# Kernel optimization log

Hardware: AMD Instinct MI355X
Metric: run time of the kernel (lower is better)

The kernel has to match this reference:

```python
import jax, jax.numpy as jnp
import numpy as np

N_NODES = 10000
N_EDGES = 80000
IN_DIM = 768
HID = 256
HEADS = 8
NEG_SLOPE = 0.2


def setup_inputs() -> dict:
    key = jax.random.key(0)
    ks = jax.random.split(key, 12)
    s = 0.02
    x = jax.random.normal(ks[0], (N_NODES, IN_DIM), dtype=jnp.float32)
    edge_index = jax.random.randint(ks[1], (2, N_EDGES), 0, N_NODES, dtype=jnp.int64)
    W1 = jax.random.normal(ks[2], (IN_DIM, HEADS * HID), dtype=jnp.float32) * s
    a_src1 = jax.random.normal(ks[3], (HEADS, HID), dtype=jnp.float32) * s
    a_dst1 = jax.random.normal(ks[4], (HEADS, HID), dtype=jnp.float32) * s
    b1 = jnp.zeros((HEADS * HID,), dtype=jnp.float32)
    W2 = jax.random.normal(ks[5], (HEADS * HID, HEADS * HID), dtype=jnp.float32) * s
    a_src2 = jax.random.normal(ks[6], (HEADS, HID), dtype=jnp.float32) * s
    a_dst2 = jax.random.normal(ks[7], (HEADS, HID), dtype=jnp.float32) * s
    b2 = jnp.zeros((HID,), dtype=jnp.float32)
    # graph_projection: 256 -> 256
    Wp = jax.random.normal(ks[8], (HID, HID), dtype=jnp.float32) * s
    bp = jnp.zeros((HID,), dtype=jnp.float32)
    return dict(x=x, edge_index=edge_index, W1=W1, a_src1=a_src1, a_dst1=a_dst1,
                b1=b1, W2=W2, a_src2=a_src2, a_dst2=a_dst2, b2=b2, Wp=Wp, bp=bp)


def _gat_conv(x, src, dst, W, a_src, a_dst, b, concat):
    """PyG GATConv (eval mode, self-loops already appended to src/dst)."""
    N = x.shape[0]
    H, C = a_src.shape
    h = (x @ W).reshape(N, H, C)                         # [N,H,C] per-head projection
    alpha_s = jnp.sum(h * a_src[None], axis=-1)           # [N,H]
    alpha_d = jnp.sum(h * a_dst[None], axis=-1)           # [N,H]
    e = jax.nn.leaky_relu(alpha_s[src] + alpha_d[dst], NEG_SLOPE)  # [E,H]
    # segment softmax over incoming edges of each dst node
    m = jax.ops.segment_max(e, dst, num_segments=N)       # [N,H]
    m = jnp.where(jnp.isfinite(m), m, 0.0)
    p = jnp.exp(e - m[dst])
    denom = jax.ops.segment_sum(p, dst, num_segments=N)   # [N,H]
    alpha = p / (denom[dst] + 1e-16)                      # [E,H]
    out = jax.ops.segment_sum(alpha[:, :, None] * h[src], dst, num_segments=N)  # [N,H,C]
    if concat:
        return out.reshape(N, H * C) + b
    return out.mean(axis=1) + b


def reference(x, edge_index, W1, a_src1, a_dst1, b1, W2, a_src2, a_dst2, b2, Wp, bp):
    N = x.shape[0]
    loops = jnp.arange(N, dtype=edge_index.dtype)
    src = jnp.concatenate([edge_index[0], loops])
    dst = jnp.concatenate([edge_index[1], loops])
    h = _gat_conv(x, src, dst, W1, a_src1, a_dst1, b1, concat=True)   # [N, 2048]
    h = jax.nn.elu(h)                                                 # dropout: eval/no-op
    h = _gat_conv(h, src, dst, W2, a_src2, a_dst2, b2, concat=False)  # [N, 256]
    h = h @ Wp + bp
    return jax.nn.relu(h)                                             # dropout: eval/no-op
```

## Files before the change

kernel.cpp:

```cpp
#include <hip/hip_runtime.h>
#include <cstdint>
#include <cstddef>

#define IN_DIM  768
#define NNODES  10000
#define MPAD    10240
#define NEDGES  80000
#define E_TOT   90000
#define HEADS   8
#define HID     256
#define HC      2048
#define NEG_SLOPE 0.2f

#define CVT_BLK  ((MPAD * IN_DIM / 4) / 256)
#define CNT_BLK  ((E_TOT + 255) / 256)
#define T1_BLK   ((HC / 32) * (IN_DIM / 32))
#define T2_BLK   ((HC / 32) * (HC / 32))
#define TP_BLK   ((HID / 32) * (HID / 32))
#define PREP_BLK (CVT_BLK + CNT_BLK + T1_BLK + T2_BLK + TP_BLK)

typedef _Float16 __attribute__((ext_vector_type(8))) f16x8;
typedef float    __attribute__((ext_vector_type(4))) f32x4;

__device__ __forceinline__ int edge_src(const int* __restrict__ ei, int e) {
    return (e < NEDGES) ? ei[e] : (e - NEDGES);
}
__device__ __forceinline__ int edge_dst(const int* __restrict__ ei, int e) {
    return (e < NEDGES) ? ei[NEDGES + e] : (e - NEDGES);
}

__device__ __forceinline__ void tcvt_body(
    const float* __restrict__ W, _Float16* __restrict__ T,
    int K, int N, int bx, int by, int t)
{
    __shared__ float tile[32][33];
    int tx = t & 31, ty = t >> 5;
#pragma unroll
    for (int q = 0; q < 4; q++)
        tile[ty + q * 8][tx] = W[(size_t)(by * 32 + ty + q * 8) * N + bx * 32 + tx];
    __syncthreads();
#pragma unroll
    for (int q = 0; q < 4; q++) {
        float v = tile[tx][ty + q * 8];
        T[(size_t)(bx * 32 + ty + q * 8) * K + by * 32 + tx] = (_Float16)v;
    }
}

__global__ __launch_bounds__(256) void prep_kernel(
    const float* __restrict__ x, _Float16* __restrict__ xh,
    const int* __restrict__ ei, int* __restrict__ cnt,
    const float* __restrict__ W1, _Float16* __restrict__ W1t,
    const float* __restrict__ W2, _Float16* __restrict__ W2t,
    const float* __restrict__ Wp, _Float16* __restrict__ Wpt)
{
    int b = blockIdx.x;
    int t = threadIdx.x;
    if (b < CVT_BLK) {
        int i = b * 256 + t;
        size_t e = (size_t)i * 4;
        int r = (int)(e / IN_DIM);
        float4 v = (r < NNODES) ? *(const float4*)(x + e)
                                : make_float4(0.f, 0.f, 0.f, 0.f);
        _Float16 h4[4] = {(_Float16)v.x, (_Float16)v.y, (_Float16)v.z, (_Float16)v.w};
        *(ushort4*)(xh + e) = *(ushort4*)h4;
    } else if (b < CVT_BLK + CNT_BLK) {
        int e = (b - CVT_BLK) * 256 + t;
        if (e < E_TOT) atomicAdd(&cnt[edge_dst(ei, e)], 1);
    } else if (b < CVT_BLK + CNT_BLK + T1_BLK) {
        int idx = b - (CVT_BLK + CNT_BLK);
        tcvt_body(W1, W1t, IN_DIM, HC, idx % (HC / 32), idx / (HC / 32), t);
    } else if (b < CVT_BLK + CNT_BLK + T1_BLK + T2_BLK) {
        int idx = b - (CVT_BLK + CNT_BLK + T1_BLK);
        tcvt_body(W2, W2t, HC, HC, idx % (HC / 32), idx / (HC / 32), t);
    } else {
        int idx = b - (CVT_BLK + CNT_BLK + T1_BLK + T2_BLK);
        tcvt_body(Wp, Wpt, HID, HID, idx % (HID / 32), idx / (HID / 32), t);
    }
}

__global__ void scan_kernel(const int* __restrict__ cnt, int* __restrict__ indptr) {
    __shared__ int sums[1024];
    const int CH = 10;
    int t = threadIdx.x;
    int base = t * CH;
    int s = 0;
#pragma unroll
    for (int i = 0; i < CH; i++) { int idx = base + i; if (idx < NNODES) s += cnt[idx]; }
    sums[t] = s;
    __syncthreads();
    for (int off = 1; off < 1024; off <<= 1) {
        int v = (t >= off) ? sums[t - off] : 0;
        __syncthreads();
        sums[t] += v;
        __syncthreads();
    }
    int run = (t == 0) ? 0 : sums[t - 1];
#pragma unroll
    for (int i = 0; i < CH; i++) {
        int idx = base + i;
        if (idx < NNODES) { indptr[idx] = run; run += cnt[idx]; }
    }
    if (t == 0) indptr[NNODES] = E_TOT;
}

__global__ void scatter_kernel(const int* __restrict__ ei, const int* __restrict__ indptr,
                               int* __restrict__ cur, int* __restrict__ sorted) {
    int e = blockIdx.x * 256 + threadIdx.x;
    if (e < E_TOT) {
        int d = edge_dst(ei, e);
        int pos = atomicAdd(&cur[d], 1);
        sorted[indptr[d] + pos] = e;
    }
}

__global__ __launch_bounds__(512, 2) void gemm8p_kernel(
    const _Float16* __restrict__ A, const _Float16* __restrict__ B,
    _Float16* __restrict__ C, int M, int K, int Nn)
{
    __shared__ __align__(16) _Float16 lds[2][36864];

    const int t = threadIdx.x;
    const int w = t >> 6, lane = t & 63;
    const int fr = lane & 15, q4 = lane >> 4;
    const int wr = w >> 2, wc = w & 3;

    const int nwgx = gridDim.x;
    int wg = blockIdx.y * nwgx + blockIdx.x;
    const int cpx = (nwgx * gridDim.y) >> 3;
    wg = (wg & 7) * cpx + (wg >> 3);
    const int row0 = (wg / nwgx) * 320;
    const int col0 = (wg % nwgx) * 256;

    const int rowt = t >> 3;
    const int scol = ((t & 7) ^ (rowt & 7)) << 3;
    const _Float16* baseA = A + (size_t)(row0 + rowt) * K + scol;
    const _Float16* baseB = B + (size_t)(col0 + rowt) * K + scol;
    const int dstw = w * 512;

    auto stageA = [&](int q, int kel, int bb) {
        __builtin_amdgcn_global_load_lds(
            (const __attribute__((address_space(1))) void*)(baseA + (size_t)q * 64 * K + kel),
            (__attribute__((address_space(3))) void*)&lds[bb][q * 4096 + dstw], 16, 0, 0);
    };
    auto stageB = [&](int q, int kel, int bb) {
        __builtin_amdgcn_global_load_lds(
            (const __attribute__((address_space(1))) void*)(baseB + (size_t)q * 64 * K + kel),
            (__attribute__((address_space(3))) void*)&lds[bb][20480 + q * 4096 + dstw], 16, 0, 0);
    };

    f32x4 acc[2][2][5][2];
#pragma unroll
    for (int qm = 0; qm < 2; qm++)
#pragma unroll
        for (int qn = 0; qn < 2; qn++)
#pragma unroll
            for (int mi = 0; mi < 5; mi++)
#pragma unroll
                for (int ni = 0; ni < 2; ni++)
                    acc[qm][qn][mi][ni] = {0.f, 0.f, 0.f, 0.f};

    f16x8 fa[5][2], fb[2][2];

#define LOADA(BB, QM)                                                           \
    {                                                                           \
        _Pragma("unroll")                                                       \
        for (int mi = 0; mi < 5; mi++) {                                        \
            _Pragma("unroll")                                                   \
            for (int ks = 0; ks < 2; ks++) {                                    \
                int lr = wr * 80 + mi * 16 + fr;                                \
                int sl = ((ks << 2) | q4) ^ (fr & 7);                           \
                fa[mi][ks] = *(const f16x8*)&lds[BB][(QM) * 10240 + (lr << 6) + (sl << 3)]; \
            }                                                                   \
        }                                                                       \
    }
#define LOADB(BB, QN)                                                           \
    {                                                                           \
        _Pragma("unroll")                                                       \
        for (int ni = 0; ni < 2; ni++) {                                        \
            _Pragma("unroll")                                                   \
            for (int ks = 0; ks < 2; ks++) {                                    \
                int lr = wc * 32 + ni * 16 + fr;                                \
                int sl = ((ks << 2) | q4) ^ (fr & 7);                           \
                fb[ni][ks] = *(const f16x8*)&lds[BB][20480 + (QN) * 8192 + (lr << 6) + (sl << 3)]; \
            }                                                                   \
        }                                                                       \
    }

#define PHASE(QM, QN, LOAD_STMT, STAGE_STMT, WAIT_STMT)                         \
    do {                                                                        \
        WAIT_STMT;                                                              \
        __builtin_amdgcn_s_barrier();                                           \
        LOAD_STMT;                                                              \
        STAGE_STMT;                                                             \
        asm volatile("s_waitcnt lgkmcnt(0)" ::: "memory");                      \
        __builtin_amdgcn_sched_barrier(0);                                      \
        __builtin_amdgcn_s_setprio(1);                                          \
        _Pragma("unroll")                                                       \
        for (int ks = 0; ks < 2; ks++) {                                        \
            _Pragma("unroll")                                                   \
            for (int mi = 0; mi < 5; mi++) {                                    \
                _Pragma("unroll")                                               \
                for (int ni = 0; ni < 2; ni++)                                  \
                    acc[QM][QN][mi][ni] = __builtin_amdgcn_mfma_f32_16x16x32_f16(\
                        fa[mi][ks], fb[ni][ks], acc[QM][QN][mi][ni], 0, 0, 0);  \
            }                                                                   \
        }                                                                       \
        __builtin_amdgcn_s_setprio(0);                                          \
        __builtin_amdgcn_sched_barrier(0);                                      \
    } while (0)

#define VM(N) asm volatile("s_waitcnt vmcnt(" #N ")" ::: "memory")

    stageA(0, 0, 0); stageA(1, 0, 0); stageA(2, 0, 0);
    stageB(0, 0, 0); stageB(1, 0, 0);
    stageB(2, 0, 0); stageB(3, 0, 0);
    stageA(3, 0, 0); stageA(4, 0, 0);

    const int nT = K >> 6;
    int t0 = 0;
    for (; t0 < nT - 1; ++t0) {
        int bb = t0 & 1;
        int bn = bb ^ 1;
        int k1 = (t0 + 1) << 6;
        PHASE(0, 0, { LOADA(bb, 0); LOADB(bb, 0); },
              { stageA(0, k1, bn); stageA(1, k1, bn); stageA(2, k1, bn); },
              VM(4));
        PHASE(0, 1, { LOADB(bb, 1); },
              { stageB(0, k1, bn); stageB(1, k1, bn); },
              VM(5));
        PHASE(1, 1, { LOADA(bb, 1); },
              { stageB(2, k1, bn); stageB(3, k1, bn); },
              VM(5));
        PHASE(1, 0, { LOADB(bb, 0); },
              { stageA(3, k1, bn); stageA(4, k1, bn); },
              ((void)0));
    }
    {
        int bb = t0 & 1;
        PHASE(0, 0, { LOADA(bb, 0); LOADB(bb, 0); }, ((void)0), VM(4));
        PHASE(0, 1, { LOADB(bb, 1); },               ((void)0), VM(2));
        PHASE(1, 1, { LOADA(bb, 1); },               ((void)0), VM(0));
        PHASE(1, 0, { LOADB(bb, 0); },               ((void)0), ((void)0));
    }
#undef PHASE
#undef LOADA
#undef LOADB
#undef VM

#pragma unroll
    for (int qm = 0; qm < 2; qm++)
#pragma unroll
        for (int qn = 0; qn < 2; qn++)
#pragma unroll
            for (int mi = 0; mi < 5; mi++) {
                int mb = row0 + qm * 160 + wr * 80 + mi * 16 + q4 * 4;
#pragma unroll
                for (int ni = 0; ni < 2; ni++) {
                    int n = col0 + qn * 128 + wc * 32 + ni * 16 + fr;
#pragma unroll
                    for (int r = 0; r < 4; r++) {
                        int m = mb + r;
                        if (m < M) C[(size_t)m * Nn + n] = (_Float16)acc[qm][qn][mi][ni][r];
                    }
                }
            }
}

template <int EPI>
__global__ __launch_bounds__(256) void mfma_gemm_kernel(
    const _Float16* __restrict__ A, const _Float16* __restrict__ B,
    void* __restrict__ Cout, const float* __restrict__ bias,
    int M, int K, int Nn, int swz)
{
    __shared__ __align__(16) _Float16 sA[2][128 * 32];
    __shared__ __align__(16) _Float16 sB[2][128 * 32];

    int t = threadIdx.x;
    int bx = blockIdx.x, by = blockIdx.y;
    if (swz) {
        int id = by * 16 + bx;
        int xcd = id & 7, slot = id >> 3;
        bx = 2 * xcd + (slot & 1);
        by = slot >> 1;
    }
    int row0 = by * 128;
    int col0 = bx * 128;

    int s0 = t, s1 = t + 256;
    int m0 = s0 >> 2, k0 = (s0 & 3) * 8;
    int m1 = s1 >> 2, k1 = (s1 & 3) * 8;
    const _Float16* a0 = A + (size_t)(row0 + m0) * K + k0;
    const _Float16* a1 = A + (size_t)(row0 + m1) * K + k1;
    const _Float16* b0 = B + (size_t)(col0 + m0) * K + k0;
    const _Float16* b1 = B + (size_t)(col0 + m1) * K + k1;

    int w = t >> 6, lane = t & 63;
    int wm = (w & 1) * 64, wn = (w >> 1) * 64;
    int fr = lane & 15, quad = lane >> 4;

    auto stage = [&](int kt, int bsel) {
        _Float16* dA0 = &sA[bsel][(w * 64) * 8];
        _Float16* dA1 = &sA[bsel][(w * 64 + 256) * 8];
        _Float16* dB0 = &sB[bsel][(w * 64) * 8];
        _Float16* dB1 = &sB[bsel][(w * 64 + 256) * 8];
        __builtin_amdgcn_global_load_lds(
            (const __attribute__((address_space(1))) void*)(a0 + kt),
            (__attribute__((address_space(3))) void*)dA0, 16, 0, 0);
        __builtin_amdgcn_global_load_lds(
            (const __attribute__((address_space(1))) void*)(a1 + kt),
            (__attribute__((address_space(3))) void*)dA1, 16, 0, 0);
        __builtin_amdgcn_global_load_lds(
            (const __attribute__((address_space(1))) void*)(b0 + kt),
            (__attribute__((address_space(3))) void*)dB0, 16, 0, 0);
        __builtin_amdgcn_global_load_lds(
            (const __attribute__((address_space(1))) void*)(b1 + kt),
            (__attribute__((address_space(3))) void*)dB1, 16, 0, 0);
    };

    f32x4 acc[4][4];
#pragma unroll
    for (int i = 0; i < 4; i++)
#pragma unroll
        for (int j = 0; j < 4; j++) acc[i][j] = {0.f, 0.f, 0.f, 0.f};

    const int nIt = K / 32;
    stage(0, 0);
    __syncthreads();

    for (int it = 0; it < nIt; ++it) {
        int cb = it & 1;
        if (it + 1 < nIt) stage((it + 1) * 32, cb ^ 1);

        f16x8 fa[4], fb[4];
#pragma unroll
        for (int i = 0; i < 4; i++) {
            fa[i] = *(const f16x8*)&sA[cb][(wm + i * 16 + fr) * 32 + quad * 8];
            fb[i] = *(const f16x8*)&sB[cb][(wn + i * 16 + fr) * 32 + quad * 8];
        }
#pragma unroll
        for (int i = 0; i < 4; i++)
#pragma unroll
            for (int j = 0; j < 4; j++)
                acc[i][j] = __builtin_amdgcn_mfma_f32_16x16x32_f16(fa[i], fb[j], acc[i][j], 0, 0, 0);

        if (it + 1 < nIt) __syncthreads();
    }

    if (EPI == 0) {
        _Float16* C = (_Float16*)Cout;
#pragma unroll
        for (int i = 0; i < 4; i++) {
            int mbase = row0 + wm + i * 16 + quad * 4;
#pragma unroll
            for (int j = 0; j < 4; j++) {
                int n = col0 + wn + j * 16 + fr;
#pragma unroll
                for (int r = 0; r < 4; r++) {
                    int m = mbase + r;
                    if (m < M) C[(size_t)m * Nn + n] = (_Float16)acc[i][j][r];
                }
            }
        }
    } else {
        float* C = (float*)Cout;
        float bv[4];
#pragma unroll
        for (int j = 0; j < 4; j++) bv[j] = bias[col0 + wn + j * 16 + fr];
#pragma unroll
        for (int i = 0; i < 4; i++) {
            int mbase = row0 + wm + i * 16 + quad * 4;
#pragma unroll
            for (int j = 0; j < 4; j++) {
                int n = col0 + wn + j * 16 + fr;
#pragma unroll
                for (int r = 0; r < 4; r++) {
                    int m = mbase + r;
                    if (m < M) C[(size_t)m * Nn + n] = fmaxf(acc[i][j][r] + bv[j], 0.f);
                }
            }
        }
    }
}

__global__ __launch_bounds__(256) void attn_kernel(
    const _Float16* __restrict__ H, const float* __restrict__ a_src,
    const float* __restrict__ a_dst, float* __restrict__ as_out,
    float* __restrict__ ad_out)
{
    int n = blockIdx.x;
    int t = threadIdx.x;
    int h = t >> 5, l = t & 31;
    f16x8 hv = *(const f16x8*)&H[(size_t)n * HC + h * HID + l * 8];
    const float* asp = a_src + h * HID + l * 8;
    const float* adp = a_dst + h * HID + l * 8;
    float sa = 0.f, sd = 0.f;
#pragma unroll
    for (int q = 0; q < 8; q++) {
        float v = (float)hv[q];
        sa = fmaf(v, asp[q], sa);
        sd = fmaf(v, adp[q], sd);
    }
#pragma unroll
    for (int o = 16; o > 0; o >>= 1) {
        sa += __shfl_xor(sa, o, 32);
        sd += __shfl_xor(sd, o, 32);
    }
    if (l == 0) { as_out[n * HEADS + h] = sa; ad_out[n * HEADS + h] = sd; }
}

template <int MODE>
__global__ __launch_bounds__(256) void agg_kernel(
    const _Float16* __restrict__ H, const float* __restrict__ as_,
    const float* __restrict__ ad_, const float* __restrict__ bias,
    const int* __restrict__ indptr, const int* __restrict__ sorted,
    const int* __restrict__ ei, _Float16* __restrict__ outh)
{
    __shared__ float m8[HEADS], d8[HEADS], adl[HEADS];
    __shared__ int   srcl[64];
    __shared__ float al[64][HEADS];
    __shared__ float red[HC];

    int n = blockIdx.x;
    int t = threadIdx.x;

    if (n >= NNODES) {
        if (MODE == 0) {
            _Float16 z8[8] = {};
            *(f16x8*)&outh[(size_t)n * HC + t * 8] = *(f16x8*)z8;
        } else {
            outh[(size_t)n * HID + t] = (_Float16)0.f;
        }
        return;
    }

    int start = indptr[n];
    int deg = indptr[n + 1] - start;

    if (t < HEADS) adl[t] = ad_[n * HEADS + t];
    __syncthreads();

    int h = t >> 5, l = t & 31;
    float adh = adl[h];

    float mx = -1e30f;
    for (int j = l; j < deg; j += 32) {
        int e = sorted[start + j];
        int s = edge_src(ei, e);
        float v = as_[s * HEADS + h] + adh;
        v = (v >= 0.f) ? v : NEG_SLOPE * v;
        mx = fmaxf(mx, v);
    }
#pragma unroll
    for (int o = 16; o > 0; o >>= 1) mx = fmaxf(mx, __shfl_xor(mx, o, 32));

    float sm = 0.f;
    for (int j = l; j < deg; j += 32) {
        int e = sorted[start + j];
        int s = edge_src(ei, e);
        float v = as_[s * HEADS + h] + adh;
        v = (v >= 0.f) ? v : NEG_SLOPE * v;
        sm += expf(v - mx);
    }
#pragma unroll
    for (int o = 16; o > 0; o >>= 1) sm += __shfl_xor(sm, o, 32);
    if (l == 0) { m8[h] = mx; d8[h] = sm; }

    int hh = t >> 5, c8 = (t & 31) * 8;
    const size_t hoff = (size_t)hh * HID + c8;
    float acc[8] = {};
    for (int base = 0; base < deg; base += 64) {
        int cntc = min(64, deg - base);
        __syncthreads();
        if (t < cntc) srcl[t] = edge_src(ei, sorted[start + base + t]);
        __syncthreads();
        {
            int j = t & 63, h0 = t >> 6;
            if (j < cntc) {
#pragma unroll
                for (int q = 0; q < 2; q++) {
                    int hx = h0 + q * 4;
                    float v = as_[srcl[j] * HEADS + hx] + adl[hx];
                    v = (v >= 0.f) ? v : NEG_SLOPE * v;
                    al[j][hx] = expf(v - m8[hx]) / (d8[hx] + 1e-16f);
                }
            }
        }
        __syncthreads();
        int jj = 0;
        for (; jj + 3 < cntc; jj += 4) {
            int sx0 = srcl[jj + 0], sx1 = srcl[jj + 1];
            int sx2 = srcl[jj + 2], sx3 = srcl[jj + 3];
            f16x8 h0v = *(const f16x8*)&H[(size_t)sx0 * HC + hoff];
            f16x8 h1v = *(const f16x8*)&H[(size_t)sx1 * HC + hoff];
            f16x8 h2v = *(const f16x8*)&H[(size_t)sx2 * HC + hoff];
            f16x8 h3v = *(const f16x8*)&H[(size_t)sx3 * HC + hoff];
            float a0 = al[jj + 0][hh], a1 = al[jj + 1][hh];
            float a2 = al[jj + 2][hh], a3 = al[jj + 3][hh];
#pragma unroll
            for (int q = 0; q < 8; q++) acc[q] = fmaf(a0, (float)h0v[q], acc[q]);
#pragma unroll
            for (int q = 0; q < 8; q++) acc[q] = fmaf(a1, (float)h1v[q], acc[q]);
#pragma unroll
            for (int q = 0; q < 8; q++) acc[q] = fmaf(a2, (float)h2v[q], acc[q]);
#pragma unroll
            for (int q = 0; q < 8; q++) acc[q] = fmaf(a3, (float)h3v[q], acc[q]);
        }
        for (; jj < cntc; jj++) {
            int s = srcl[jj];
            f16x8 hv = *(const f16x8*)&H[(size_t)s * HC + hoff];
            float a = al[jj][hh];
#pragma unroll
            for (int q = 0; q < 8; q++)
                acc[q] = fmaf(a, (float)hv[q], acc[q]);
        }
    }

    if (MODE == 0) {
        _Float16 o8[8];
#pragma unroll
        for (int q = 0; q < 8; q++) {
            float v = acc[q] + bias[hoff + q];
            v = (v > 0.f) ? v : expm1f(v);
            o8[q] = (_Float16)v;
        }
        *(f16x8*)&outh[(size_t)n * HC + hoff] = *(f16x8*)o8;
    } else {
#pragma unroll
        for (int q = 0; q < 8; q++) red[hoff + q] = acc[q];
        __syncthreads();
        float s = 0.f;
#pragma unroll
        for (int h2 = 0; h2 < HEADS; h2++) s += red[h2 * HID + t];
        outh[(size_t)n * HID + t] = (_Float16)(s * 0.125f + bias[t]);
    }
}

extern "C" void kernel_launch(void* const* d_in, const int* in_sizes, int n_in,
                              void* d_out, int out_size, void* d_ws, size_t ws_size,
                              hipStream_t stream)
{
    const float* x      = (const float*)d_in[0];
    const int*   ei     = (const int*)  d_in[1];
    const float* W1     = (const float*)d_in[2];
    const float* a_src1 = (const float*)d_in[3];
    const float* a_dst1 = (const float*)d_in[4];
    const float* b1     = (const float*)d_in[5];
    const float* W2     = (const float*)d_in[6];
    const float* a_src2 = (const float*)d_in[7];
    const float* a_dst2 = (const float*)d_in[8];
    const float* b2     = (const float*)d_in[9];
    const float* Wp     = (const float*)d_in[10];
    const float* bp     = (const float*)d_in[11];
    float* out = (float*)d_out;

    char* ws = (char*)d_ws;
    size_t off = 0;
    auto alloc = [&](size_t bytes) -> char* {
        char* p = ws + off;
        off += (bytes + 255) & ~(size_t)255;
        return p;
    };
    _Float16* Hbuf = (_Float16*)alloc((size_t)NNODES * HC * 2);
    _Float16* A2   = (_Float16*)alloc((size_t)MPAD * HC * 2);
    _Float16* W1t  = (_Float16*)alloc((size_t)HC * IN_DIM * 2);
    _Float16* W2t  = (_Float16*)alloc((size_t)HC * HC * 2);
    _Float16* Wpt  = (_Float16*)alloc((size_t)HID * HID * 2);
    _Float16* xh   = (_Float16*)alloc((size_t)MPAD * IN_DIM * 2);
    _Float16* out2h = (_Float16*)alloc((size_t)MPAD * HID * 2);
    float* asad   = (float*)alloc((size_t)4 * NNODES * HEADS * sizeof(float));
    float* as1 = asad;
    float* ad1 = asad + (size_t)NNODES * HEADS;
    float* as2 = asad + (size_t)2 * NNODES * HEADS;
    float* ad2 = asad + (size_t)3 * NNODES * HEADS;
    int*   cntcur = (int*)alloc((size_t)2 * NNODES * sizeof(int));
    int*   cnt = cntcur;
    int*   cur = cntcur + NNODES;
    int*   indptr = (int*)  alloc((size_t)(NNODES + 1) * sizeof(int));
    int*   sorted = (int*)  alloc((size_t)E_TOT * sizeof(int));

    hipMemsetAsync(cntcur, 0, (size_t)2 * NNODES * sizeof(int), stream);
    prep_kernel<<<PREP_BLK, 256, 0, stream>>>(x, xh, ei, cnt,
                                              W1, W1t, W2, W2t, Wp, Wpt);
    scan_kernel<<<1, 1024, 0, stream>>>(cnt, indptr);
    scatter_kernel<<<(E_TOT + 255) / 256, 256, 0, stream>>>(ei, indptr, cur, sorted);

    dim3 g8(HC / 256, MPAD / 320);

    gemm8p_kernel<<<g8, 512, 0, stream>>>(xh, W1t, Hbuf, NNODES, IN_DIM, HC);
    attn_kernel<<<NNODES, 256, 0, stream>>>(Hbuf, a_src1, a_dst1, as1, ad1);
    agg_kernel<0><<<MPAD, 256, 0, stream>>>(Hbuf, as1, ad1, b1, indptr, sorted, ei, A2);

    gemm8p_kernel<<<g8, 512, 0, stream>>>(A2, W2t, Hbuf, NNODES, HC, HC);
    attn_kernel<<<NNODES, 256, 0, stream>>>(Hbuf, a_src2, a_dst2, as2, ad2);
    agg_kernel<1><<<MPAD, 256, 0, stream>>>(Hbuf, as2, ad2, b2, indptr, sorted, ei, out2h);

    dim3 gProj(HID / 128, MPAD / 128);
    mfma_gemm_kernel<1><<<gProj, 256, 0, stream>>>(out2h, Wpt, out, bp,
                                                   NNODES, HID, HID, 0);
}
```

Measured before the change: 406.3 us.

## Rewrite GAT aggregation as wave-per-node and adjust GEMM LDS scheduling

The aggregation kernel moves from one 256-thread block per node to one 64-lane wavefront per node, four nodes per block. Each lane computes all 8 heads' softmax weights for one edge and broadcasts source ids with shuffles, which removes most block-level syncthreads and the LDS reduction. The scatter kernel now stores source node ids directly, so the aggregation no longer does an extra index indirection. Separately, the GEMM phase drops the explicit lgkmcnt wait and setprio and reorders its LDS fragment loads, leaving wait placement to the compiler, which may change how loads overlap with MFMA.

Result: slower. 417.4 us (+2.7%).

```diff
diff --git a/kernel.cpp b/kernel.cpp
--- a/kernel.cpp
+++ b/kernel.cpp
@@ -109,7 +109,7 @@
     if (e < E_TOT) {
         int d = edge_dst(ei, e);
         int pos = atomicAdd(&cur[d], 1);
-        sorted[indptr[d] + pos] = e;
+        sorted[indptr[d] + pos] = edge_src(ei, e);
     }
 }
 
@@ -164,9 +164,9 @@
 #define LOADA(BB, QM)                                                           \
     {                                                                           \
         _Pragma("unroll")                                                       \
-        for (int mi = 0; mi < 5; mi++) {                                        \
+        for (int ks = 0; ks < 2; ks++) {                                        \
             _Pragma("unroll")                                                   \
-            for (int ks = 0; ks < 2; ks++) {                                    \
+            for (int mi = 0; mi < 5; mi++) {                                    \
                 int lr = wr * 80 + mi * 16 + fr;                                \
                 int sl = ((ks << 2) | q4) ^ (fr & 7);                           \
                 fa[mi][ks] = *(const f16x8*)&lds[BB][(QM) * 10240 + (lr << 6) + (sl << 3)]; \
@@ -176,9 +176,9 @@
 #define LOADB(BB, QN)                                                           \
     {                                                                           \
         _Pragma("unroll")                                                       \
-        for (int ni = 0; ni < 2; ni++) {                                        \
+        for (int ks = 0; ks < 2; ks++) {                                        \
             _Pragma("unroll")                                                   \
-            for (int ks = 0; ks < 2; ks++) {                                    \
+            for (int ni = 0; ni < 2; ni++) {                                    \
                 int lr = wc * 32 + ni * 16 + fr;                                \
                 int sl = ((ks << 2) | q4) ^ (fr & 7);                           \
                 fb[ni][ks] = *(const f16x8*)&lds[BB][20480 + (QN) * 8192 + (lr << 6) + (sl << 3)]; \
@@ -190,11 +190,9 @@
     do {                                                                        \
         WAIT_STMT;                                                              \
         __builtin_amdgcn_s_barrier();                                           \
+        __builtin_amdgcn_sched_barrier(0);                                      \
         LOAD_STMT;                                                              \
         STAGE_STMT;                                                             \
-        asm volatile("s_waitcnt lgkmcnt(0)" ::: "memory");                      \
-        __builtin_amdgcn_sched_barrier(0);                                      \
-        __builtin_amdgcn_s_setprio(1);                                          \
         _Pragma("unroll")                                                       \
         for (int ks = 0; ks < 2; ks++) {                                        \
             _Pragma("unroll")                                                   \
@@ -205,8 +203,6 @@
                         fa[mi][ks], fb[ni][ks], acc[QM][QN][mi][ni], 0, 0, 0);  \
             }                                                                   \
         }                                                                       \
-        __builtin_amdgcn_s_setprio(0);                                          \
-        __builtin_amdgcn_sched_barrier(0);                                      \
     } while (0)
 
 #define VM(N) asm volatile("s_waitcnt vmcnt(" #N ")" ::: "memory")
@@ -413,125 +409,201 @@
     const _Float16* __restrict__ H, const float* __restrict__ as_,
     const float* __restrict__ ad_, const float* __restrict__ bias,
     const int* __restrict__ indptr, const int* __restrict__ sorted,
-    const int* __restrict__ ei, _Float16* __restrict__ outh)
+    _Float16* __restrict__ outh)
 {
-    __shared__ float m8[HEADS], d8[HEADS], adl[HEADS];
-    __shared__ int   srcl[64];
-    __shared__ float al[64][HEADS];
-    __shared__ float red[HC];
-
-    int n = blockIdx.x;
-    int t = threadIdx.x;
+    __shared__ float alw[4][8][64];
+
+    const int t = threadIdx.x;
+    const int w = t >> 6, lane = t & 63;
+    const int n = blockIdx.x * 4 + w;
 
     if (n >= NNODES) {
+        _Float16 z8[8] = {};
         if (MODE == 0) {
-            _Float16 z8[8] = {};
-            *(f16x8*)&outh[(size_t)n * HC + t * 8] = *(f16x8*)z8;
+#pragma unroll
+            for (int c = 0; c < 4; c++)
+                *(f16x8*)&outh[(size_t)n * HC + c * 512 + lane * 8] = *(f16x8*)z8;
         } else {
-            outh[(size_t)n * HID + t] = (_Float16)0.f;
+            if (lane < 32)
+                *(f16x8*)&outh[(size_t)n * HID + lane * 8] = *(f16x8*)z8;
         }
         return;
     }
 
-    int start = indptr[n];
-    int deg = indptr[n + 1] - start;
-
-    if (t < HEADS) adl[t] = ad_[n * HEADS + t];
-    __syncthreads();
-
-    int h = t >> 5, l = t & 31;
-    float adh = adl[h];
-
-    float mx = -1e30f;
-    for (int j = l; j < deg; j += 32) {
-        int e = sorted[start + j];
-        int s = edge_src(ei, e);
-        float v = as_[s * HEADS + h] + adh;
-        v = (v >= 0.f) ? v : NEG_SLOPE * v;
-        mx = fmaxf(mx, v);
-    }
-#pragma unroll
-    for (int o = 16; o > 0; o >>= 1) mx = fmaxf(mx, __shfl_xor(mx, o, 32));
-
-    float sm = 0.f;
-    for (int j = l; j < deg; j += 32) {
-        int e = sorted[start + j];
-        int s = edge_src(ei, e);
-        float v = as_[s * HEADS + h] + adh;
-        v = (v >= 0.f) ? v : NEG_SLOPE * v;
-        sm += expf(v - mx);
-    }
-#pragma unroll
-    for (int o = 16; o > 0; o >>= 1) sm += __shfl_xor(sm, o, 32);
-    if (l == 0) { m8[h] = mx; d8[h] = sm; }
-
-    int hh = t >> 5, c8 = (t & 31) * 8;
-    const size_t hoff = (size_t)hh * HID + c8;
-    float acc[8] = {};
-    for (int base = 0; base < deg; base += 64) {
-        int cntc = min(64, deg - base);
-        __syncthreads();
-        if (t < cntc) srcl[t] = edge_src(ei, sorted[start + base + t]);
-        __syncthreads();
-        {
-            int j = t & 63, h0 = t >> 6;
-            if (j < cntc) {
-#pragma unroll
-                for (int q = 0; q < 2; q++) {
-                    int hx = h0 + q * 4;
-                    float v = as_[srcl[j] * HEADS + hx] + adl[hx];
+    const int start = indptr[n];
+    const int deg = indptr[n + 1] - start;
+
+    float4 dd0 = *(const float4*)&ad_[n * HEADS];
+    float4 dd1 = *(const float4*)&ad_[n * HEADS + 4];
+    const float ad8[8] = {dd0.x, dd0.y, dd0.z, dd0.w, dd1.x, dd1.y, dd1.z, dd1.w};
+
+    float acc[4][8];
+#pragma unroll
+    for (int c = 0; c < 4; c++)
+#pragma unroll
+        for (int q = 0; q < 8; q++) acc[c][q] = 0.f;
+
+    const int hp = lane >> 5;
+    float* alme = &alw[w][0][0];
+
+    if (deg <= 64) {
+        int s_l = 0;
+        float p[8];
+        if (lane < deg) {
+            s_l = sorted[start + lane];
+            float4 a0 = *(const float4*)&as_[s_l * HEADS];
+            float4 a1 = *(const float4*)&as_[s_l * HEADS + 4];
+            float va[8] = {a0.x, a0.y, a0.z, a0.w, a1.x, a1.y, a1.z, a1.w};
+#pragma unroll
+            for (int h = 0; h < 8; h++) {
+                float v = va[h] + ad8[h];
+                p[h] = (v >= 0.f) ? v : NEG_SLOPE * v;
+            }
+        } else {
+#pragma unroll
+            for (int h = 0; h < 8; h++) p[h] = -1e30f;
+        }
+#pragma unroll
+        for (int h = 0; h < 8; h++) {
+            float mx = p[h];
+#pragma unroll
+            for (int o = 32; o > 0; o >>= 1) mx = fmaxf(mx, __shfl_xor(mx, o, 64));
+            float e = (lane < deg) ? expf(p[h] - mx) : 0.f;
+            float sm = e;
+#pragma unroll
+            for (int o = 32; o > 0; o >>= 1) sm += __shfl_xor(sm, o, 64);
+            alme[h * 64 + lane] = e / (sm + 1e-16f);
+        }
+        asm volatile("s_waitcnt lgkmcnt(0)" ::: "memory");
+
+        int jj = 0;
+        for (; jj + 1 < deg; jj += 2) {
+            int s0 = __shfl(s_l, jj, 64);
+            int s1 = __shfl(s_l, jj + 1, 64);
+            const _Float16* r0 = &H[(size_t)s0 * HC + lane * 8];
+            const _Float16* r1 = &H[(size_t)s1 * HC + lane * 8];
+            f16x8 h0[4], h1[4];
+#pragma unroll
+            for (int c = 0; c < 4; c++) h0[c] = *(const f16x8*)(r0 + c * 512);
+#pragma unroll
+            for (int c = 0; c < 4; c++) h1[c] = *(const f16x8*)(r1 + c * 512);
+#pragma unroll
+            for (int c = 0; c < 4; c++) {
+                float a0 = alme[(2 * c + hp) * 64 + jj];
+                float a1v = alme[(2 * c + hp) * 64 + jj + 1];
+#pragma unroll
+                for (int q = 0; q < 8; q++) acc[c][q] = fmaf(a0, (float)h0[c][q], acc[c][q]);
+#pragma unroll
+                for (int q = 0; q < 8; q++) acc[c][q] = fmaf(a1v, (float)h1[c][q], acc[c][q]);
+            }
+        }
+        if (jj < deg) {
+            int s0 = __shfl(s_l, jj, 64);
+            const _Float16* r0 = &H[(size_t)s0 * HC + lane * 8];
+#pragma unroll
+            for (int c = 0; c < 4; c++) {
+                f16x8 hv = *(const f16x8*)(r0 + c * 512);
+                float a0 = alme[(2 * c + hp) * 64 + jj];
+#pragma unroll
+                for (int q = 0; q < 8; q++) acc[c][q] = fmaf(a0, (float)hv[q], acc[c][q]);
+            }
+        }
+    } else {
+        float mx8[8], sm8[8];
+#pragma unroll
+        for (int h = 0; h < 8; h++) { mx8[h] = -1e30f; sm8[h] = 0.f; }
+        for (int j = lane; j < deg; j += 64) {
+            int s = sorted[start + j];
+            float4 a0 = *(const float4*)&as_[s * HEADS];
+            float4 a1 = *(const float4*)&as_[s * HEADS + 4];
+            float va[8] = {a0.x, a0.y, a0.z, a0.w, a1.x, a1.y, a1.z, a1.w};
+#pragma unroll
+            for (int h = 0; h < 8; h++) {
+                float v = va[h] + ad8[h];
+                v = (v >= 0.f) ? v : NEG_SLOPE * v;
+                mx8[h] = fmaxf(mx8[h], v);
+            }
+        }
+#pragma unroll
+        for (int h = 0; h < 8; h++)
+#pragma unroll
+            for (int o = 32; o > 0; o >>= 1) mx8[h] = fmaxf(mx8[h], __shfl_xor(mx8[h], o, 64));
+        for (int j = lane; j < deg; j += 64) {
+            int s = sorted[start + j];
+            float4 a0 = *(const float4*)&as_[s * HEADS];
+            float4 a1 = *(const float4*)&as_[s * HEADS + 4];
+            float va[8] = {a0.x, a0.y, a0.z, a0.w, a1.x, a1.y, a1.z, a1.w};
+#pragma unroll
+            for (int h = 0; h < 8; h++) {
+                float v = va[h] + ad8[h];
+                v = (v >= 0.f) ? v : NEG_SLOPE * v;
+                sm8[h] += expf(v - mx8[h]);
+            }
+        }
+#pragma unroll
+        for (int h = 0; h < 8; h++) {
+#pragma unroll
+            for (int o = 32; o > 0; o >>= 1) sm8[h] += __shfl_xor(sm8[h], o, 64);
+            sm8[h] += 1e-16f;
+        }
+        for (int base = 0; base < deg; base += 64) {
+            int cnt = min(64, deg - base);
+            int s_l = 0;
+            if (lane < cnt) {
+                s_l = sorted[start + base + lane];
+                float4 a0 = *(const float4*)&as_[s_l * HEADS];
+                float4 a1 = *(const float4*)&as_[s_l * HEADS + 4];
+                float va[8] = {a0.x, a0.y, a0.z, a0.w, a1.x, a1.y, a1.z, a1.w};
+#pragma unroll
+                for (int h = 0; h < 8; h++) {
+                    float v = va[h] + ad8[h];
                     v = (v >= 0.f) ? v : NEG_SLOPE * v;
-                    al[j][hx] = expf(v - m8[hx]) / (d8[hx] + 1e-16f);
+                    alme[h * 64 + lane] = expf(v - mx8[h]) / sm8[h];
                 }
             }
-        }
-        __syncthreads();
-        int jj = 0;
-        for (; jj + 3 < cntc; jj += 4) {
-            int sx0 = srcl[jj + 0], sx1 = srcl[jj + 1];
-            int sx2 = srcl[jj + 2], sx3 = srcl[jj + 3];
-            f16x8 h0v = *(const f16x8*)&H[(size_t)sx0 * HC + hoff];
-            f16x8 h1v = *(const f16x8*)&H[(size_t)sx1 * HC + hoff];
-            f16x8 h2v = *(const f16x8*)&H[(size_t)sx2 * HC + hoff];
-            f16x8 h3v = *(const f16x8*)&H[(size_t)sx3 * HC + hoff];
-            float a0 = al[jj + 0][hh], a1 = al[jj + 1][hh];
-            float a2 = al[jj + 2][hh], a3 = al[jj + 3][hh];
-#pragma unroll
-            for (int q = 0; q < 8; q++) acc[q] = fmaf(a0, (float)h0v[q], acc[q]);
-#pragma unroll
-            for (int q = 0; q < 8; q++) acc[q] = fmaf(a1, (float)h1v[q], acc[q]);
-#pragma unroll
-            for (int q = 0; q < 8; q++) acc[q] = fmaf(a2, (float)h2v[q], acc[q]);
-#pragma unroll
-            for (int q = 0; q < 8; q++) acc[q] = fmaf(a3, (float)h3v[q], acc[q]);
-        }
-        for (; jj < cntc; jj++) {
-            int s = srcl[jj];
-            f16x8 hv = *(const f16x8*)&H[(size_t)s * HC + hoff];
-            float a = al[jj][hh];
+            asm volatile("s_waitcnt lgkmcnt(0)" ::: "memory");
+            for (int jj = 0; jj < cnt; jj++) {
+                int s0 = __shfl(s_l, jj, 64);
+                const _Float16* r0 = &H[(size_t)s0 * HC + lane * 8];
+#pragma unroll
+                for (int c = 0; c < 4; c++) {
+                    f16x8 hv = *(const f16x8*)(r0 + c * 512);
+                    float a0 = alme[(2 * c + hp) * 64 + jj];
+#pragma unroll
+                    for (int q = 0; q < 8; q++) acc[c][q] = fmaf(a0, (float)hv[q], acc[c][q]);
+                }
+            }
+            asm volatile("s_waitcnt lgkmcnt(0)" ::: "memory");
+        }
+    }
+
+    if (MODE == 0) {
+#pragma unroll
+        for (int c = 0; c < 4; c++) {
+            _Float16 o8[8];
+#pragma unroll
+            for (int q = 0; q < 8; q++) {
+                float v = acc[c][q] + bias[c * 512 + lane * 8 + q];
+                v = (v > 0.f) ? v : expm1f(v);
+                o8[q] = (_Float16)v;
+            }
+            *(f16x8*)&outh[(size_t)n * HC + c * 512 + lane * 8] = *(f16x8*)o8;
+        }
+    } else {
+        float s8[8];
+#pragma unroll
+        for (int q = 0; q < 8; q++)
+            s8[q] = acc[0][q] + acc[1][q] + acc[2][q] + acc[3][q];
+#pragma unroll
+        for (int q = 0; q < 8; q++) s8[q] += __shfl_xor(s8[q], 32, 64);
+        if (lane < 32) {
+            int d0i = lane * 8;
+            _Float16 o8[8];
 #pragma unroll
             for (int q = 0; q < 8; q++)
-                acc[q] = fmaf(a, (float)hv[q], acc[q]);
-        }
-    }
-
-    if (MODE == 0) {
-        _Float16 o8[8];
-#pragma unroll
-        for (int q = 0; q < 8; q++) {
-            float v = acc[q] + bias[hoff + q];
-            v = (v > 0.f) ? v : expm1f(v);
-            o8[q] = (_Float16)v;
-        }
-        *(f16x8*)&outh[(size_t)n * HC + hoff] = *(f16x8*)o8;
-    } else {
-#pragma unroll
-        for (int q = 0; q < 8; q++) red[hoff + q] = acc[q];
-        __syncthreads();
-        float s = 0.f;
-#pragma unroll
-        for (int h2 = 0; h2 < HEADS; h2++) s += red[h2 * HID + t];
-        outh[(size_t)n * HID + t] = (_Float16)(s * 0.125f + bias[t]);
+                o8[q] = (_Float16)(s8[q] * 0.125f + bias[d0i + q]);
+            *(f16x8*)&outh[(size_t)n * HID + d0i] = *(f16x8*)o8;
+        }
     }
 }
 
@@ -588,11 +660,11 @@
 
     gemm8p_kernel<<<g8, 512, 0, stream>>>(xh, W1t, Hbuf, NNODES, IN_DIM, HC);
     attn_kernel<<<NNODES, 256, 0, stream>>>(Hbuf, a_src1, a_dst1, as1, ad1);
-    agg_kernel<0><<<MPAD, 256, 0, stream>>>(Hbuf, as1, ad1, b1, indptr, sorted, ei, A2);
+    agg_kernel<0><<<MPAD / 4, 256, 0, stream>>>(Hbuf, as1, ad1, b1, indptr, sorted, A2);
 
     gemm8p_kernel<<<g8, 512, 0, stream>>>(A2, W2t, Hbuf, NNODES, HC, HC);
     attn_kernel<<<NNODES, 256, 0, stream>>>(Hbuf, a_src2, a_dst2, as2, ad2);
-    agg_kernel<1><<<MPAD, 256, 0, stream>>>(Hbuf, as2, ad2, b2, indptr, sorted, ei, out2h);
+    agg_kernel<1><<<MPAD / 4, 256, 0, stream>>>(Hbuf, as2, ad2, b2, indptr, sorted, out2h);
 
     dim3 gProj(HID / 128, MPAD / 128);
     mfma_gemm_kernel<1><<<gProj, 256, 0, stream>>>(out2h, Wpt, out, bp,
```
